# Kernel optimization log

Measured on AMD Instinct MI355X. Metric: run time of the kernel, lower is better.

The kernel has to match this reference:

```python
import jax, jax.numpy as jnp
import numpy as np

B, L, D, H = 2, 2048, 2048, 16
HD = D // H           # head_dim = 128
HD2 = HD // 2         # rotary pair count = 64


def setup_inputs() -> dict:
    key = jax.random.key(0)
    ks = jax.random.split(key, 6)
    x = jax.random.normal(ks[0], (B, L, D), dtype=jnp.float32)
    # RoPE angles: theta_i = 10000^(-2i/HD), angles[l, i] = l * theta_i
    inv_freq = 1.0 / (10000.0 ** (np.arange(0, HD, 2, dtype=np.float32) / HD))
    angles = np.arange(L, dtype=np.float32)[:, None] * inv_freq[None, :]  # [L, HD2]
    freqs_cos = jnp.asarray(np.cos(angles))[None]  # [1, L, HD2]
    freqs_sin = jnp.asarray(np.sin(angles))[None]  # [1, L, HD2]
    s = 1.0 / np.sqrt(D)
    Wq = jax.random.normal(ks[1], (D, D), dtype=jnp.float32) * s
    Wk = jax.random.normal(ks[2], (D, D), dtype=jnp.float32) * s
    Wv = jax.random.normal(ks[3], (D, D), dtype=jnp.float32) * s
    Wo = jax.random.normal(ks[4], (D, D), dtype=jnp.float32) * s
    return {"x": x, "freqs_cos": freqs_cos, "freqs_sin": freqs_sin,
            "Wq": Wq, "Wk": Wk, "Wv": Wv, "Wo": Wo}


def _apply_rope(t, cos, sin):
    # t: [B, H, L, HD]; cos/sin: [1, L, HD2] -> broadcast as [1, 1, L, HD2]
    t2 = t.reshape(*t.shape[:-1], HD2, 2)
    t0, t1 = t2[..., 0], t2[..., 1]
    c = cos[:, None]
    s = sin[:, None]
    r0 = t0 * c - t1 * s
    r1 = t0 * s + t1 * c
    return jnp.stack([r0, r1], axis=-1).reshape(t.shape)


def reference(x, freqs_cos, freqs_sin, Wq, Wk, Wv, Wo):
    b, l, d = x.shape
    # projections (torch Linear: x @ W.T)
    Q = (x @ Wq.T).reshape(b, l, H, HD).transpose(0, 2, 1, 3)  # [b,h,l,hd]
    K = (x @ Wk.T).reshape(b, l, H, HD).transpose(0, 2, 1, 3)
    V = (x @ Wv.T).reshape(b, l, H, HD).transpose(0, 2, 1, 3)
    Q = _apply_rope(Q, freqs_cos[:, :l], freqs_sin[:, :l])
    K = _apply_rope(K, freqs_cos[:, :l], freqs_sin[:, :l])
    scale = 1.0 / jnp.sqrt(jnp.asarray(HD, dtype=x.dtype))
    scores = jnp.einsum('bhqd,bhkd->bhqk', Q, K) * scale  # [b,h,l,l]
    causal = jnp.tril(jnp.ones((l, l), dtype=bool))
    scores = jnp.where(causal, scores, jnp.finfo(scores.dtype).min)
    probs = jax.nn.softmax(scores, axis=-1)
    out = jnp.einsum('bhqk,bhkd->bhqd', probs, V)  # [b,h,l,hd]
    out = out.transpose(0, 2, 1, 3).reshape(b, l, d)
    return out @ Wo.T
```

## Files before the change

kernel.cpp:

```cpp
#include <hip/hip_runtime.h>
#include <cstdint>
#include <cstddef>

typedef float f32x4 __attribute__((ext_vector_type(4)));
typedef short bf16x8 __attribute__((ext_vector_type(8)));
typedef short bf16x4 __attribute__((ext_vector_type(4)));
typedef unsigned int u32x4 __attribute__((ext_vector_type(4)));

#define LOG2E 1.4426950408889634f
#define K2E 0.12750102296293331f
#define MFMA_BF16 __builtin_amdgcn_mfma_f32_16x16x32_bf16

__device__ inline float bf2f(short s) {
  return (float)__builtin_bit_cast(__bf16, s);
}
__device__ inline short f2bf(float f) {
  return __builtin_bit_cast(short, (__bf16)f);
}
__device__ inline unsigned f2bfu(float f) {
  return (unsigned)__builtin_bit_cast(unsigned short, (__bf16)f);
}

__device__ inline void gload_lds16(const void* g, void* l) {
  __builtin_amdgcn_global_load_lds(
      (const __attribute__((address_space(1))) void*)g,
      (__attribute__((address_space(3))) void*)l, 16, 0, 0);
}

__global__ __launch_bounds__(256) void cvt_bf16(const float* __restrict__ in,
                                                __bf16* __restrict__ out, int n) {
  int i = (blockIdx.x * 256 + threadIdx.x) * 8;
  if (i >= n) return;
  f32x4 a = *(const f32x4*)(in + i);
  f32x4 b = *(const f32x4*)(in + i + 4);
  bf16x8 r;
#pragma unroll
  for (int j = 0; j < 4; ++j) {
    r[j]     = f2bf(a[j]);
    r[j + 4] = f2bf(b[j]);
  }
  *(bf16x8*)(out + i) = r;
}

__device__ inline void stage_half(const __bf16* __restrict__ gbase, int K,
                                  int k0, char* ldsHalf, int wid, int lane) {
#pragma unroll
  for (int j = 0; j < 2; ++j) {
    int idx = (wid * 2 + j) * 64 + lane;
    int row = idx >> 3;
    int c16 = (idx & 7) ^ (row & 7);
    gload_lds16(gbase + (size_t)row * K + k0 + c16 * 8,
                ldsHalf + (wid * 2 + j) * 1024);
  }
}

__device__ inline bf16x8 lds_frag(const char* halfbase, int row, int ks, int g) {
  return *(const bf16x8*)(halfbase + row * 128 + ((((ks << 2) | g) ^ (row & 7)) << 4));
}

#define WAITV(n) asm volatile("s_waitcnt vmcnt(" #n ")" ::: "memory")

template <bool OUT_F32>
__global__ __launch_bounds__(512, 1) void gemm128(const __bf16* __restrict__ A,
                                                  const __bf16* __restrict__ B,
                                                  void* __restrict__ Cv,
                                                  int M, int N, int K) {
  __shared__ __attribute__((aligned(128))) char lds[147456];
  const int tid = threadIdx.x, wid = tid >> 6, lane = tid & 63;
  const int g = lane >> 4, lc = lane & 15;
  const int wm = wid >> 2, wn = wid & 3;

  const int gx = gridDim.x;
  int nwg = gx * gridDim.y;
  int bid = blockIdx.y * gx + blockIdx.x;
  int cpx = nwg >> 3;
  int swz = (bid & 7) * cpx + (bid >> 3);
  const int bx = swz % gx, by = swz / gx;

  const __bf16* Ag = A + (size_t)(by * 128) * K;
  const __bf16* Bg = B + (size_t)(bx * 256) * K;
  const __bf16* Bg1 = Bg + 128 * (size_t)K;
  const int NT = K >> 6;

  f32x4 acc[2][4][2];
#pragma unroll
  for (int hb = 0; hb < 2; ++hb)
#pragma unroll
    for (int m = 0; m < 4; ++m)
#pragma unroll
      for (int n = 0; n < 2; ++n) acc[hb][m][n] = f32x4{0.f, 0.f, 0.f, 0.f};

  stage_half(Ag,  K, 0,  lds + 0,             wid, lane);
  stage_half(Bg,  K, 0,  lds + 49152,         wid, lane);
  stage_half(Bg1, K, 0,  lds + 98304,         wid, lane);
  stage_half(Ag,  K, 64, lds + 16384,         wid, lane);
  stage_half(Bg,  K, 64, lds + 49152 + 16384, wid, lane);
  stage_half(Bg1, K, 64, lds + 98304 + 16384, wid, lane);
  WAITV(8);
  __builtin_amdgcn_s_barrier();

  bf16x8 a[4][2], b0[2][2], b1[2][2];
  int sc = 0;

  for (int T = 0; T < NT; ++T) {
    char* As  = lds + sc * 16384;
    char* B0s = lds + 49152 + sc * 16384;
    char* B1s = lds + 98304 + sc * 16384;
    int s2 = sc + 2; if (s2 >= 3) s2 -= 3;
    char* As2  = lds + s2 * 16384;
    char* B0s2 = lds + 49152 + s2 * 16384;
    char* B1s2 = lds + 98304 + s2 * 16384;
    const int k2 = (T + 2) << 6;

#pragma unroll
    for (int m = 0; m < 4; ++m)
#pragma unroll
      for (int ks = 0; ks < 2; ++ks)
        a[m][ks] = lds_frag(As, wm * 64 + m * 16 + lc, ks, g);
#pragma unroll
    for (int n = 0; n < 2; ++n)
#pragma unroll
      for (int ks = 0; ks < 2; ++ks)
        b0[n][ks] = lds_frag(B0s, wn * 32 + n * 16 + lc, ks, g);
    if (T + 2 < NT) {
      stage_half(Ag, K, k2, As2, wid, lane);
      stage_half(Bg, K, k2, B0s2, wid, lane);
      WAITV(10);
    } else if (T + 1 < NT) {
      WAITV(6);
    } else {
      WAITV(0);
    }
    __builtin_amdgcn_s_barrier();
    __builtin_amdgcn_s_setprio(1);
#pragma unroll
    for (int m = 0; m < 4; ++m)
#pragma unroll
      for (int n = 0; n < 2; ++n) {
        acc[0][m][n] = MFMA_BF16(a[m][0], b0[n][0], acc[0][m][n], 0, 0, 0);
        acc[0][m][n] = MFMA_BF16(a[m][1], b0[n][1], acc[0][m][n], 0, 0, 0);
      }
    __builtin_amdgcn_s_setprio(0);

#pragma unroll
    for (int n = 0; n < 2; ++n)
#pragma unroll
      for (int ks = 0; ks < 2; ++ks)
        b1[n][ks] = lds_frag(B1s, wn * 32 + n * 16 + lc, ks, g);
    if (T + 2 < NT) {
      stage_half(Bg1, K, k2, B1s2, wid, lane);
      WAITV(8);
    } else if (T + 1 < NT) {
      WAITV(2);
    }
    __builtin_amdgcn_s_barrier();
    __builtin_amdgcn_s_setprio(1);
#pragma unroll
    for (int m = 0; m < 4; ++m)
#pragma unroll
      for (int n = 0; n < 2; ++n) {
        acc[1][m][n] = MFMA_BF16(a[m][0], b1[n][0], acc[1][m][n], 0, 0, 0);
        acc[1][m][n] = MFMA_BF16(a[m][1], b1[n][1], acc[1][m][n], 0, 0, 0);
      }
    __builtin_amdgcn_s_setprio(0);

    sc = (sc + 1 == 3) ? 0 : sc + 1;
  }

#pragma unroll
  for (int hb = 0; hb < 2; ++hb)
#pragma unroll
    for (int m = 0; m < 4; ++m)
#pragma unroll
      for (int n = 0; n < 2; ++n)
#pragma unroll
        for (int r = 0; r < 4; ++r) {
          int rr = by * 128 + wm * 64 + m * 16 + g * 4 + r;
          int cc = bx * 256 + hb * 128 + wn * 32 + n * 16 + lc;
          if (OUT_F32)
            ((float*)Cv)[(size_t)rr * N + cc] = acc[hb][m][n][r];
          else
            ((__bf16*)Cv)[(size_t)rr * N + cc] = (__bf16)acc[hb][m][n][r];
        }
}

__global__ __launch_bounds__(256) void rope_kernel(__bf16* __restrict__ qkv,
                                                   const float* __restrict__ fc,
                                                   const float* __restrict__ fs) {
  int idx = blockIdx.x * 256 + threadIdx.x;
  int row = idx >> 9;
  int col = (idx & 511) * 8;
  int l = row & 2047;
  int i0 = (col & 127) >> 1;
  __bf16* p = qkv + (size_t)row * 6144 + col;
  bf16x8 v = *(const bf16x8*)p;
  f32x4 c4 = *(const f32x4*)(fc + l * 64 + i0);
  f32x4 s4 = *(const f32x4*)(fs + l * 64 + i0);
  bf16x8 r;
#pragma unroll
  for (int j = 0; j < 4; ++j) {
    float t0 = bf2f(v[2 * j]), t1 = bf2f(v[2 * j + 1]);
    r[2 * j]     = f2bf(t0 * c4[j] - t1 * s4[j]);
    r[2 * j + 1] = f2bf(t0 * s4[j] + t1 * c4[j]);
  }
  *(bf16x8*)p = r;
}

__global__ void transpose_v(const __bf16* __restrict__ qkv, __bf16* __restrict__ vt) {
  __shared__ __bf16 tile[32][33];
  const int b = blockIdx.z;
  const int l0 = blockIdx.x * 32, c0 = blockIdx.y * 32;
  for (int i = threadIdx.y; i < 32; i += 8)
    tile[i][threadIdx.x] = qkv[(size_t)(b * 2048 + l0 + i) * 6144 + 4096 + c0 + threadIdx.x];
  __syncthreads();
  for (int i = threadIdx.y; i < 32; i += 8)
    vt[(size_t)b * 4194304 + (size_t)(c0 + i) * 2048 + l0 + threadIdx.x] = tile[threadIdx.x][i];
}

__device__ __forceinline__ void attn_segment(const __bf16* __restrict__ qkv,
                                             const __bf16* __restrict__ vt,
                                             __bf16* __restrict__ aout,
                                             int b, int h, int bh,
                                             int qseg0, int nt,
                                             char* Ks, char* Vs, int tid) {
  const int wid = tid >> 6, lane = tid & 63;
  const int g = lane >> 4, lc = lane & 15;
  const int q0w = qseg0 + wid * 16;
  const float k2e = K2E;

  bf16x8 qreg[4];
  {
    const __bf16* qp = qkv + (size_t)(b * 2048 + q0w + lc) * 6144 + h * 128 + g * 8;
#pragma unroll
    for (int c = 0; c < 4; ++c) qreg[c] = *(const bf16x8*)(qp + c * 32);
  }

  f32x4 oaccT[8];
#pragma unroll
  for (int dc = 0; dc < 8; ++dc) oaccT[dc] = f32x4{0.f, 0.f, 0.f, 0.f};
  float m_run = -1e30f, l_run = 0.f;

  const int rK = tid >> 2, sK = tid & 3;
  const int dbase = tid >> 3, sg = tid & 7;
  const __bf16* kb = qkv + (size_t)(b * 2048) * 6144 + 2048 + h * 128;
  const __bf16* vb = vt + (size_t)bh * 262144;

  bf16x8 kreg[4], vreg[4];
  {
    const __bf16* kg = kb + (size_t)rK * 6144 + sK * 8;
#pragma unroll
    for (int kk = 0; kk < 4; ++kk) kreg[kk] = *(const bf16x8*)(kg + kk * 32);
    const __bf16* vg = vb + sg * 8;
#pragma unroll
    for (int kk = 0; kk < 4; ++kk)
      vreg[kk] = *(const bf16x8*)(vg + (size_t)(dbase + kk * 32) * 2048);
  }

  for (int t = 0; t < nt; ++t) {
    const int kv0 = t * 64;
    __syncthreads();
#pragma unroll
    for (int kk = 0; kk < 4; ++kk)
      *(bf16x8*)(Ks + rK * 256 + ((sK * 16 + kk * 64) ^ ((rK & 7) << 4))) = kreg[kk];
#pragma unroll
    for (int kk = 0; kk < 4; ++kk) {
      int d = dbase + kk * 32;
      *(bf16x8*)(Vs + d * 128 + ((sg * 16) ^ ((d & 7) << 4))) = vreg[kk];
    }
    __syncthreads();

    if (t + 1 < nt) {
      const __bf16* kg = kb + (size_t)(kv0 + 64 + rK) * 6144 + sK * 8;
#pragma unroll
      for (int kk = 0; kk < 4; ++kk) kreg[kk] = *(const bf16x8*)(kg + kk * 32);
      const __bf16* vg = vb + kv0 + 64 + sg * 8;
#pragma unroll
      for (int kk = 0; kk < 4; ++kk)
        vreg[kk] = *(const bf16x8*)(vg + (size_t)(dbase + kk * 32) * 2048);
    }

    f32x4 sacc[4];
#pragma unroll
    for (int kc = 0; kc < 4; ++kc) sacc[kc] = f32x4{0.f, 0.f, 0.f, 0.f};
#pragma unroll
    for (int kc = 0; kc < 4; ++kc) {
      const int kr = kc * 16 + lc;
#pragma unroll
      for (int c = 0; c < 4; ++c) {
        bf16x8 kf = *(const bf16x8*)(Ks + kr * 256 + ((c * 64 + g * 16) ^ ((kr & 7) << 4)));
        sacc[kc] = MFMA_BF16(kf, qreg[c], sacc[kc], 0, 0, 0);
      }
    }

    if (kv0 + 63 > q0w) {
#pragma unroll
      for (int kc = 0; kc < 4; ++kc)
#pragma unroll
        for (int r = 0; r < 4; ++r)
          if (kv0 + kc * 16 + g * 4 + r > q0w + lc) sacc[kc][r] = -1e30f;
    }

    float mx = sacc[0][0];
#pragma unroll
    for (int kc = 0; kc < 4; ++kc)
#pragma unroll
      for (int r = 0; r < 4; ++r) mx = fmaxf(mx, sacc[kc][r]);
    mx = fmaxf(mx, __shfl_xor(mx, 16));
    mx = fmaxf(mx, __shfl_xor(mx, 32));
    float mn = fmaxf(m_run, mx);
    float al = exp2f((m_run - mn) * k2e);
    m_run = mn;
    float p[4][4];
    float ls = 0.f;
#pragma unroll
    for (int kc = 0; kc < 4; ++kc)
#pragma unroll
      for (int r = 0; r < 4; ++r) {
        p[kc][r] = exp2f((sacc[kc][r] - mn) * k2e);
        ls += p[kc][r];
      }
    ls += __shfl_xor(ls, 16);
    ls += __shfl_xor(ls, 32);
    l_run = l_run * al + ls;
#pragma unroll
    for (int dc = 0; dc < 8; ++dc)
#pragma unroll
      for (int r = 0; r < 4; ++r) oaccT[dc][r] *= al;

    unsigned pk[4][2];
#pragma unroll
    for (int kc = 0; kc < 4; ++kc)
#pragma unroll
      for (int hh = 0; hh < 2; ++hh)
        pk[kc][hh] = f2bfu(p[kc][2 * hh]) | (f2bfu(p[kc][2 * hh + 1]) << 16);

    const int sA = (g & 1) * 32 + lc, sB = sA + 16;
    const bool hi = (g >> 1) != 0;
    bf16x8 brg[2];
#pragma unroll
    for (int c = 0; c < 2; ++c) {
      unsigned a0 = (unsigned)__shfl((int)pk[2 * c][0], sA);
      unsigned b0v = (unsigned)__shfl((int)pk[2 * c + 1][0], sA);
      unsigned a1 = (unsigned)__shfl((int)pk[2 * c][1], sA);
      unsigned b1v = (unsigned)__shfl((int)pk[2 * c + 1][1], sA);
      unsigned a2 = (unsigned)__shfl((int)pk[2 * c][0], sB);
      unsigned b2v = (unsigned)__shfl((int)pk[2 * c + 1][0], sB);
      unsigned a3 = (unsigned)__shfl((int)pk[2 * c][1], sB);
      unsigned b3v = (unsigned)__shfl((int)pk[2 * c + 1][1], sB);
      u32x4 wv;
      wv[0] = hi ? b0v : a0;
      wv[1] = hi ? b1v : a1;
      wv[2] = hi ? b2v : a2;
      wv[3] = hi ? b3v : a3;
      brg[c] = __builtin_bit_cast(bf16x8, wv);
    }

#pragma unroll
    for (int dc = 0; dc < 8; ++dc) {
      const int vr = dc * 16 + lc;
      bf16x8 vf0 = *(const bf16x8*)(Vs + vr * 128 + ((g * 16) ^ ((vr & 7) << 4)));
      bf16x8 vf1 = *(const bf16x8*)(Vs + vr * 128 + ((64 + g * 16) ^ ((vr & 7) << 4)));
      oaccT[dc] = MFMA_BF16(vf0, brg[0], oaccT[dc], 0, 0, 0);
      oaccT[dc] = MFMA_BF16(vf1, brg[1], oaccT[dc], 0, 0, 0);
    }
  }

  {
    float inv = 1.f / l_run;
    __bf16* op = aout + (size_t)(b * 2048 + q0w + lc) * 2048 + h * 128 + g * 4;
#pragma unroll
    for (int dc = 0; dc < 8; ++dc) {
      bf16x4 o;
#pragma unroll
      for (int r = 0; r < 4; ++r) o[r] = f2bf(oaccT[dc][r] * inv);
      *(bf16x4*)(op + dc * 16) = o;
    }
  }
}

__global__ __launch_bounds__(256, 2) void flash_attn(const __bf16* __restrict__ qkv,
                                                     const __bf16* __restrict__ vt,
                                                     __bf16* __restrict__ aout) {
  __shared__ __attribute__((aligned(16))) char smem[32768];
  char* Ks = smem;
  char* Vs = smem + 16384;
  const int tid = threadIdx.x;
  const int j = blockIdx.x;
  const int bh = blockIdx.y, b = bh >> 4, h = bh & 15;

  attn_segment(qkv, vt, aout, b, h, bh, j * 64, j + 1, Ks, Vs, tid);
  attn_segment(qkv, vt, aout, b, h, bh, (31 - j) * 64, 32 - j, Ks, Vs, tid);
}

extern "C" void kernel_launch(void* const* d_in, const int* in_sizes, int n_in,
                              void* d_out, int out_size, void* d_ws, size_t ws_size,
                              hipStream_t stream) {
  const float* x    = (const float*)d_in[0];
  const float* fcos = (const float*)d_in[1];
  const float* fsin = (const float*)d_in[2];
  const float* Wq   = (const float*)d_in[3];
  const float* Wk   = (const float*)d_in[4];
  const float* Wv   = (const float*)d_in[5];
  const float* Wo   = (const float*)d_in[6];

  char* ws = (char*)d_ws;
  __bf16* xb   = (__bf16*)(ws);
  __bf16* Wqkv = (__bf16*)(ws + 16777216);
  __bf16* Wob  = (__bf16*)(ws + 41943040);
  __bf16* QKV  = (__bf16*)(ws + 50331648);
  __bf16* Vt   = (__bf16*)(ws + 100663296);
  __bf16* aout = (__bf16*)(ws + 117440512);
  float* out = (float*)d_out;

  cvt_bf16<<<4096, 256, 0, stream>>>(x, xb, 8388608);
  cvt_bf16<<<2048, 256, 0, stream>>>(Wq, Wqkv, 4194304);
  cvt_bf16<<<2048, 256, 0, stream>>>(Wk, Wqkv + 4194304, 4194304);
  cvt_bf16<<<2048, 256, 0, stream>>>(Wv, Wqkv + 8388608, 4194304);
  cvt_bf16<<<2048, 256, 0, stream>>>(Wo, Wob, 4194304);

  gemm128<false><<<dim3(24, 32), 512, 0, stream>>>(xb, Wqkv, QKV, 4096, 6144, 2048);
  rope_kernel<<<8192, 256, 0, stream>>>(QKV, fcos, fsin);
  transpose_v<<<dim3(64, 64, 2), dim3(32, 8), 0, stream>>>(QKV, Vt);
  flash_attn<<<dim3(16, 32), 256, 0, stream>>>(QKV, Vt, aout);
  gemm128<true><<<dim3(8, 32), 512, 0, stream>>>(aout, Wob, out, 4096, 2048, 2048);
}
```

Measured before the change: 286.1 us.

## Fuse RoPE into QKV GEMM epilogue, merge weight casts, widen attention per-wave tiles

Applies RoPE inside the QKV GEMM epilogue using lane shuffles, which removes the separate rope kernel and its read/write pass over Q and K. The four weight conversions are merged into one launch that writes Wo contiguously after Wqkv. Flash attention now runs 128 threads per block with each wave handling 32 query rows (two 16-row fragments), so each K/V fragment read from LDS is reused across both. This halves the number of waves per block and raises register pressure per wave.

New measurement: 470.4 us. +64.4%, slower.

```diff
diff --git a/kernel.cpp b/kernel.cpp
--- a/kernel.cpp
+++ b/kernel.cpp
@@ -42,6 +42,26 @@
   *(bf16x8*)(out + i) = r;
 }
 
+__global__ __launch_bounds__(256) void cvt_w4(const float* __restrict__ w0,
+                                              const float* __restrict__ w1,
+                                              const float* __restrict__ w2,
+                                              const float* __restrict__ w3,
+                                              __bf16* __restrict__ out) {
+  int i = (blockIdx.x * 256 + threadIdx.x) * 8;
+  int sel = i >> 22;
+  const float* s = (sel == 0) ? w0 : (sel == 1) ? w1 : (sel == 2) ? w2 : w3;
+  int off = i & 4194303;
+  f32x4 a = *(const f32x4*)(s + off);
+  f32x4 b = *(const f32x4*)(s + off + 4);
+  bf16x8 r;
+#pragma unroll
+  for (int j = 0; j < 4; ++j) {
+    r[j]     = f2bf(a[j]);
+    r[j + 4] = f2bf(b[j]);
+  }
+  *(bf16x8*)(out + i) = r;
+}
+
 __device__ inline void stage_half(const __bf16* __restrict__ gbase, int K,
                                   int k0, char* ldsHalf, int wid, int lane) {
 #pragma unroll
@@ -60,10 +80,12 @@
 
 #define WAITV(n) asm volatile("s_waitcnt vmcnt(" #n ")" ::: "memory")
 
-template <bool OUT_F32>
+template <bool OUT_F32, bool ROPE>
 __global__ __launch_bounds__(512, 1) void gemm128(const __bf16* __restrict__ A,
                                                   const __bf16* __restrict__ B,
                                                   void* __restrict__ Cv,
+                                                  const float* __restrict__ fc,
+                                                  const float* __restrict__ fs,
                                                   int M, int N, int K) {
   __shared__ __attribute__((aligned(128))) char lds[147456];
   const int tid = threadIdx.x, wid = tid >> 6, lane = tid & 63;
@@ -167,6 +189,27 @@
     sc = (sc + 1 == 3) ? 0 : sc + 1;
   }
 
+  if (ROPE && bx < 16) {
+#pragma unroll
+    for (int m = 0; m < 4; ++m)
+#pragma unroll
+      for (int r = 0; r < 4; ++r) {
+        int l = (by * 128 + wm * 64 + m * 16 + g * 4 + r) & 2047;
+#pragma unroll
+        for (int n = 0; n < 2; ++n) {
+          int i0 = (wn * 32 + n * 16 + lc) >> 1;
+          float c = fc[l * 64 + i0];
+          float s = fs[l * 64 + i0];
+#pragma unroll
+          for (int hb = 0; hb < 2; ++hb) {
+            float v = acc[hb][m][n][r];
+            float pv = __shfl_xor(v, 1);
+            acc[hb][m][n][r] = (lc & 1) ? (pv * s + v * c) : (v * c - pv * s);
+          }
+        }
+      }
+  }
+
 #pragma unroll
   for (int hb = 0; hb < 2; ++hb)
 #pragma unroll
@@ -182,28 +225,6 @@
           else
             ((__bf16*)Cv)[(size_t)rr * N + cc] = (__bf16)acc[hb][m][n][r];
         }
-}
-
-__global__ __launch_bounds__(256) void rope_kernel(__bf16* __restrict__ qkv,
-                                                   const float* __restrict__ fc,
-                                                   const float* __restrict__ fs) {
-  int idx = blockIdx.x * 256 + threadIdx.x;
-  int row = idx >> 9;
-  int col = (idx & 511) * 8;
-  int l = row & 2047;
-  int i0 = (col & 127) >> 1;
-  __bf16* p = qkv + (size_t)row * 6144 + col;
-  bf16x8 v = *(const bf16x8*)p;
-  f32x4 c4 = *(const f32x4*)(fc + l * 64 + i0);
-  f32x4 s4 = *(const f32x4*)(fs + l * 64 + i0);
-  bf16x8 r;
-#pragma unroll
-  for (int j = 0; j < 4; ++j) {
-    float t0 = bf2f(v[2 * j]), t1 = bf2f(v[2 * j + 1]);
-    r[2 * j]     = f2bf(t0 * c4[j] - t1 * s4[j]);
-    r[2 * j + 1] = f2bf(t0 * s4[j] + t1 * c4[j]);
-  }
-  *(bf16x8*)p = r;
 }
 
 __global__ void transpose_v(const __bf16* __restrict__ qkv, __bf16* __restrict__ vt) {
@@ -225,134 +246,141 @@
                                              char* Ks, char* Vs, int tid) {
   const int wid = tid >> 6, lane = tid & 63;
   const int g = lane >> 4, lc = lane & 15;
-  const int q0w = qseg0 + wid * 16;
+  const int q0 = qseg0 + wid * 32;
   const float k2e = K2E;
 
-  bf16x8 qreg[4];
-  {
-    const __bf16* qp = qkv + (size_t)(b * 2048 + q0w + lc) * 6144 + h * 128 + g * 8;
-#pragma unroll
-    for (int c = 0; c < 4; ++c) qreg[c] = *(const bf16x8*)(qp + c * 32);
-  }
-
-  f32x4 oaccT[8];
-#pragma unroll
-  for (int dc = 0; dc < 8; ++dc) oaccT[dc] = f32x4{0.f, 0.f, 0.f, 0.f};
-  float m_run = -1e30f, l_run = 0.f;
-
-  const int rK = tid >> 2, sK = tid & 3;
-  const int dbase = tid >> 3, sg = tid & 7;
+  bf16x8 qreg[2][4];
+#pragma unroll
+  for (int qf = 0; qf < 2; ++qf) {
+    const __bf16* qp = qkv + (size_t)(b * 2048 + q0 + qf * 16 + lc) * 6144 + h * 128 + g * 8;
+#pragma unroll
+    for (int c = 0; c < 4; ++c) qreg[qf][c] = *(const bf16x8*)(qp + c * 32);
+  }
+
+  f32x4 oaccT[2][8];
+#pragma unroll
+  for (int qf = 0; qf < 2; ++qf)
+#pragma unroll
+    for (int dc = 0; dc < 8; ++dc) oaccT[qf][dc] = f32x4{0.f, 0.f, 0.f, 0.f};
+  float m_run[2] = {-1e30f, -1e30f}, l_run[2] = {0.f, 0.f};
+
   const __bf16* kb = qkv + (size_t)(b * 2048) * 6144 + 2048 + h * 128;
   const __bf16* vb = vt + (size_t)bh * 262144;
 
-  bf16x8 kreg[4], vreg[4];
-  {
-    const __bf16* kg = kb + (size_t)rK * 6144 + sK * 8;
-#pragma unroll
-    for (int kk = 0; kk < 4; ++kk) kreg[kk] = *(const bf16x8*)(kg + kk * 32);
-    const __bf16* vg = vb + sg * 8;
-#pragma unroll
-    for (int kk = 0; kk < 4; ++kk)
-      vreg[kk] = *(const bf16x8*)(vg + (size_t)(dbase + kk * 32) * 2048);
+  bf16x8 kreg[8], vreg[8];
+#pragma unroll
+  for (int p = 0; p < 8; ++p) {
+    int idx = p * 128 + tid;
+    kreg[p] = *(const bf16x8*)(kb + (size_t)(idx >> 4) * 6144 + (idx & 15) * 8);
+    vreg[p] = *(const bf16x8*)(vb + (size_t)(idx >> 3) * 2048 + (idx & 7) * 8);
   }
 
   for (int t = 0; t < nt; ++t) {
     const int kv0 = t * 64;
     __syncthreads();
 #pragma unroll
-    for (int kk = 0; kk < 4; ++kk)
-      *(bf16x8*)(Ks + rK * 256 + ((sK * 16 + kk * 64) ^ ((rK & 7) << 4))) = kreg[kk];
-#pragma unroll
-    for (int kk = 0; kk < 4; ++kk) {
-      int d = dbase + kk * 32;
-      *(bf16x8*)(Vs + d * 128 + ((sg * 16) ^ ((d & 7) << 4))) = vreg[kk];
+    for (int p = 0; p < 8; ++p) {
+      int idx = p * 128 + tid;
+      int krow = idx >> 4, kch = idx & 15;
+      *(bf16x8*)(Ks + krow * 256 + ((kch * 16) ^ ((krow & 7) << 4))) = kreg[p];
+      int d = idx >> 3, sg = idx & 7;
+      *(bf16x8*)(Vs + d * 128 + ((sg * 16) ^ ((d & 7) << 4))) = vreg[p];
     }
     __syncthreads();
 
     if (t + 1 < nt) {
-      const __bf16* kg = kb + (size_t)(kv0 + 64 + rK) * 6144 + sK * 8;
-#pragma unroll
-      for (int kk = 0; kk < 4; ++kk) kreg[kk] = *(const bf16x8*)(kg + kk * 32);
-      const __bf16* vg = vb + kv0 + 64 + sg * 8;
-#pragma unroll
-      for (int kk = 0; kk < 4; ++kk)
-        vreg[kk] = *(const bf16x8*)(vg + (size_t)(dbase + kk * 32) * 2048);
-    }
-
-    f32x4 sacc[4];
-#pragma unroll
-    for (int kc = 0; kc < 4; ++kc) sacc[kc] = f32x4{0.f, 0.f, 0.f, 0.f};
+      const __bf16* kgn = kb + (size_t)(kv0 + 64) * 6144;
+      const __bf16* vgn = vb + kv0 + 64;
+#pragma unroll
+      for (int p = 0; p < 8; ++p) {
+        int idx = p * 128 + tid;
+        kreg[p] = *(const bf16x8*)(kgn + (size_t)(idx >> 4) * 6144 + (idx & 15) * 8);
+        vreg[p] = *(const bf16x8*)(vgn + (size_t)(idx >> 3) * 2048 + (idx & 7) * 8);
+      }
+    }
+
+    f32x4 sacc[2][4];
+#pragma unroll
+    for (int qf = 0; qf < 2; ++qf)
+#pragma unroll
+      for (int kc = 0; kc < 4; ++kc) sacc[qf][kc] = f32x4{0.f, 0.f, 0.f, 0.f};
 #pragma unroll
     for (int kc = 0; kc < 4; ++kc) {
       const int kr = kc * 16 + lc;
 #pragma unroll
       for (int c = 0; c < 4; ++c) {
         bf16x8 kf = *(const bf16x8*)(Ks + kr * 256 + ((c * 64 + g * 16) ^ ((kr & 7) << 4)));
-        sacc[kc] = MFMA_BF16(kf, qreg[c], sacc[kc], 0, 0, 0);
-      }
-    }
-
-    if (kv0 + 63 > q0w) {
+        sacc[0][kc] = MFMA_BF16(kf, qreg[0][c], sacc[0][kc], 0, 0, 0);
+        sacc[1][kc] = MFMA_BF16(kf, qreg[1][c], sacc[1][kc], 0, 0, 0);
+      }
+    }
+
+    if (kv0 + 63 > q0) {
+#pragma unroll
+      for (int qf = 0; qf < 2; ++qf)
+#pragma unroll
+        for (int kc = 0; kc < 4; ++kc)
+#pragma unroll
+          for (int r = 0; r < 4; ++r)
+            if (kv0 + kc * 16 + g * 4 + r > q0 + qf * 16 + lc) sacc[qf][kc][r] = -1e30f;
+    }
+
+    bf16x8 brg[2][2];
+#pragma unroll
+    for (int qf = 0; qf < 2; ++qf) {
+      float mx = sacc[qf][0][0];
 #pragma unroll
       for (int kc = 0; kc < 4; ++kc)
 #pragma unroll
-        for (int r = 0; r < 4; ++r)
-          if (kv0 + kc * 16 + g * 4 + r > q0w + lc) sacc[kc][r] = -1e30f;
-    }
-
-    float mx = sacc[0][0];
-#pragma unroll
-    for (int kc = 0; kc < 4; ++kc)
-#pragma unroll
-      for (int r = 0; r < 4; ++r) mx = fmaxf(mx, sacc[kc][r]);
-    mx = fmaxf(mx, __shfl_xor(mx, 16));
-    mx = fmaxf(mx, __shfl_xor(mx, 32));
-    float mn = fmaxf(m_run, mx);
-    float al = exp2f((m_run - mn) * k2e);
-    m_run = mn;
-    float p[4][4];
-    float ls = 0.f;
-#pragma unroll
-    for (int kc = 0; kc < 4; ++kc)
-#pragma unroll
-      for (int r = 0; r < 4; ++r) {
-        p[kc][r] = exp2f((sacc[kc][r] - mn) * k2e);
-        ls += p[kc][r];
-      }
-    ls += __shfl_xor(ls, 16);
-    ls += __shfl_xor(ls, 32);
-    l_run = l_run * al + ls;
-#pragma unroll
-    for (int dc = 0; dc < 8; ++dc)
-#pragma unroll
-      for (int r = 0; r < 4; ++r) oaccT[dc][r] *= al;
-
-    unsigned pk[4][2];
-#pragma unroll
-    for (int kc = 0; kc < 4; ++kc)
-#pragma unroll
-      for (int hh = 0; hh < 2; ++hh)
-        pk[kc][hh] = f2bfu(p[kc][2 * hh]) | (f2bfu(p[kc][2 * hh + 1]) << 16);
-
-    const int sA = (g & 1) * 32 + lc, sB = sA + 16;
-    const bool hi = (g >> 1) != 0;
-    bf16x8 brg[2];
-#pragma unroll
-    for (int c = 0; c < 2; ++c) {
-      unsigned a0 = (unsigned)__shfl((int)pk[2 * c][0], sA);
-      unsigned b0v = (unsigned)__shfl((int)pk[2 * c + 1][0], sA);
-      unsigned a1 = (unsigned)__shfl((int)pk[2 * c][1], sA);
-      unsigned b1v = (unsigned)__shfl((int)pk[2 * c + 1][1], sA);
-      unsigned a2 = (unsigned)__shfl((int)pk[2 * c][0], sB);
-      unsigned b2v = (unsigned)__shfl((int)pk[2 * c + 1][0], sB);
-      unsigned a3 = (unsigned)__shfl((int)pk[2 * c][1], sB);
-      unsigned b3v = (unsigned)__shfl((int)pk[2 * c + 1][1], sB);
-      u32x4 wv;
-      wv[0] = hi ? b0v : a0;
-      wv[1] = hi ? b1v : a1;
-      wv[2] = hi ? b2v : a2;
-      wv[3] = hi ? b3v : a3;
-      brg[c] = __builtin_bit_cast(bf16x8, wv);
+        for (int r = 0; r < 4; ++r) mx = fmaxf(mx, sacc[qf][kc][r]);
+      mx = fmaxf(mx, __shfl_xor(mx, 16));
+      mx = fmaxf(mx, __shfl_xor(mx, 32));
+      float mn = fmaxf(m_run[qf], mx);
+      float al = exp2f((m_run[qf] - mn) * k2e);
+      m_run[qf] = mn;
+      float p[4][4];
+      float ls = 0.f;
+#pragma unroll
+      for (int kc = 0; kc < 4; ++kc)
+#pragma unroll
+        for (int r = 0; r < 4; ++r) {
+          p[kc][r] = exp2f((sacc[qf][kc][r] - mn) * k2e);
+          ls += p[kc][r];
+        }
+      ls += __shfl_xor(ls, 16);
+      ls += __shfl_xor(ls, 32);
+      l_run[qf] = l_run[qf] * al + ls;
+#pragma unroll
+      for (int dc = 0; dc < 8; ++dc)
+#pragma unroll
+        for (int r = 0; r < 4; ++r) oaccT[qf][dc][r] *= al;
+
+      unsigned pk[4][2];
+#pragma unroll
+      for (int kc = 0; kc < 4; ++kc)
+#pragma unroll
+        for (int hh = 0; hh < 2; ++hh)
+          pk[kc][hh] = f2bfu(p[kc][2 * hh]) | (f2bfu(p[kc][2 * hh + 1]) << 16);
+
+      const int sA = (g & 1) * 32 + lc, sB = sA + 16;
+      const bool hi = (g >> 1) != 0;
+#pragma unroll
+      for (int c = 0; c < 2; ++c) {
+        unsigned a0 = (unsigned)__shfl((int)pk[2 * c][0], sA);
+        unsigned b0v = (unsigned)__shfl((int)pk[2 * c + 1][0], sA);
+        unsigned a1 = (unsigned)__shfl((int)pk[2 * c][1], sA);
+        unsigned b1v = (unsigned)__shfl((int)pk[2 * c + 1][1], sA);
+        unsigned a2 = (unsigned)__shfl((int)pk[2 * c][0], sB);
+        unsigned b2v = (unsigned)__shfl((int)pk[2 * c + 1][0], sB);
+        unsigned a3 = (unsigned)__shfl((int)pk[2 * c][1], sB);
+        unsigned b3v = (unsigned)__shfl((int)pk[2 * c + 1][1], sB);
+        u32x4 wv;
+        wv[0] = hi ? b0v : a0;
+        wv[1] = hi ? b1v : a1;
+        wv[2] = hi ? b2v : a2;
+        wv[3] = hi ? b3v : a3;
+        brg[qf][c] = __builtin_bit_cast(bf16x8, wv);
+      }
     }
 
 #pragma unroll
@@ -360,36 +388,39 @@
       const int vr = dc * 16 + lc;
       bf16x8 vf0 = *(const bf16x8*)(Vs + vr * 128 + ((g * 16) ^ ((vr & 7) << 4)));
       bf16x8 vf1 = *(const bf16x8*)(Vs + vr * 128 + ((64 + g * 16) ^ ((vr & 7) << 4)));
-      oaccT[dc] = MFMA_BF16(vf0, brg[0], oaccT[dc], 0, 0, 0);
-      oaccT[dc] = MFMA_BF16(vf1, brg[1], oaccT[dc], 0, 0, 0);
-    }
-  }
-
-  {
-    float inv = 1.f / l_run;
-    __bf16* op = aout + (size_t)(b * 2048 + q0w + lc) * 2048 + h * 128 + g * 4;
+      oaccT[0][dc] = MFMA_BF16(vf0, brg[0][0], oaccT[0][dc], 0, 0, 0);
+      oaccT[0][dc] = MFMA_BF16(vf1, brg[0][1], oaccT[0][dc], 0, 0, 0);
+      oaccT[1][dc] = MFMA_BF16(vf0, brg[1][0], oaccT[1][dc], 0, 0, 0);
+      oaccT[1][dc] = MFMA_BF16(vf1, brg[1][1], oaccT[1][dc], 0, 0, 0);
+    }
+  }
+
+#pragma unroll
+  for (int qf = 0; qf < 2; ++qf) {
+    float inv = 1.f / l_run[qf];
+    __bf16* op = aout + (size_t)(b * 2048 + q0 + qf * 16 + lc) * 2048 + h * 128 + g * 4;
 #pragma unroll
     for (int dc = 0; dc < 8; ++dc) {
       bf16x4 o;
 #pragma unroll
-      for (int r = 0; r < 4; ++r) o[r] = f2bf(oaccT[dc][r] * inv);
+      for (int r = 0; r < 4; ++r) o[r] = f2bf(oaccT[qf][dc][r] * inv);
       *(bf16x4*)(op + dc * 16) = o;
     }
   }
 }
 
-__global__ __launch_bounds__(256, 2) void flash_attn(const __bf16* __restrict__ qkv,
+__global__ __launch_bounds__(128, 2) void flash_attn(const __bf16* __restrict__ qkv,
                                                      const __bf16* __restrict__ vt,
                                                      __bf16* __restrict__ aout) {
   __shared__ __attribute__((aligned(16))) char smem[32768];
   char* Ks = smem;
   char* Vs = smem + 16384;
   const int tid = threadIdx.x;
-  const int j = blockIdx.x;
+  const int t = blockIdx.x;
   const int bh = blockIdx.y, b = bh >> 4, h = bh & 15;
 
-  attn_segment(qkv, vt, aout, b, h, bh, j * 64, j + 1, Ks, Vs, tid);
-  attn_segment(qkv, vt, aout, b, h, bh, (31 - j) * 64, 32 - j, Ks, Vs, tid);
+  attn_segment(qkv, vt, aout, b, h, bh, t * 64, t + 1, Ks, Vs, tid);
+  attn_segment(qkv, vt, aout, b, h, bh, (31 - t) * 64, 32 - t, Ks, Vs, tid);
 }
 
 extern "C" void kernel_launch(void* const* d_in, const int* in_sizes, int n_in,
@@ -413,14 +444,12 @@
   float* out = (float*)d_out;
 
   cvt_bf16<<<4096, 256, 0, stream>>>(x, xb, 8388608);
-  cvt_bf16<<<2048, 256, 0, stream>>>(Wq, Wqkv, 4194304);
-  cvt_bf16<<<2048, 256, 0, stream>>>(Wk, Wqkv + 4194304, 4194304);
-  cvt_bf16<<<2048, 256, 0, stream>>>(Wv, Wqkv + 8388608, 4194304);
-  cvt_bf16<<<2048, 256, 0, stream>>>(Wo, Wob, 4194304);
-
-  gemm128<false><<<dim3(24, 32), 512, 0, stream>>>(xb, Wqkv, QKV, 4096, 6144, 2048);
-  rope_kernel<<<8192, 256, 0, stream>>>(QKV, fcos, fsin);
+  cvt_w4<<<8192, 256, 0, stream>>>(Wq, Wk, Wv, Wo, Wqkv);
+
+  gemm128<false, true><<<dim3(24, 32), 512, 0, stream>>>(xb, Wqkv, QKV, fcos, fsin,
+                                                         4096, 6144, 2048);
   transpose_v<<<dim3(64, 64, 2), dim3(32, 8), 0, stream>>>(QKV, Vt);
-  flash_attn<<<dim3(16, 32), 256, 0, stream>>>(QKV, Vt, aout);
-  gemm128<true><<<dim3(8, 32), 512, 0, stream>>>(aout, Wob, out, 4096, 2048, 2048);
-}
+  flash_attn<<<dim3(16, 32), 128, 0, stream>>>(QKV, Vt, aout);
+  gemm128<true, false><<<dim3(8, 32), 512, 0, stream>>>(aout, Wob, out, nullptr, nullptr,
+                                                        4096, 2048, 2048);
+}
```
